# Kernel tuning notes

Measured on AMD Instinct MI355X. Metric: run time of the kernel, lower is better.

The kernel has to match this reference:

```python
import jax, jax.numpy as jnp
import numpy as np

B, S, D, H, L = 2, 4096, 768, 12, 12
DH = D // H
BS = 16                # block size
NB = S // BS           # 256 blocks
NR = 2                 # random blocks per middle query block
DFF = 3072
VOCAB = 50358


def layer_norm(x, s, b):
    m = x.mean(-1, keepdims=True)
    v = ((x - m) ** 2).mean(-1, keepdims=True)
    return (x - m) * jax.lax.rsqrt(v + 1e-12) * s + b


def setup_inputs() -> dict:
    key = jax.random.key(0)
    ks = jax.random.split(key, 20)
    rn = lambda k, shp: jax.random.normal(k, shp, jnp.float32) * 0.02
    # random key-block indices per middle query block, avoiding window+global blocks
    rng = np.random.default_rng(0)
    rb = np.zeros((NB - 2, NR), np.int32)
    for i in range(1, NB - 1):
        forbidden = {0, i - 1, i, i + 1, NB - 1}
        choices = np.array([b for b in range(NB) if b not in forbidden])
        rb[i - 1] = rng.choice(choices, NR, replace=False)
    return {
        "input_ids": jax.random.randint(ks[0], (B, S), 0, VOCAB, jnp.int32),
        "rand_blocks": jnp.asarray(rb),
        "emb_word": rn(ks[1], (VOCAB, D)),
        "emb_pos": rn(ks[2], (S, D)),
        "ln0_s": jnp.ones((D,)), "ln0_b": jnp.zeros((D,)),
        "Wq": rn(ks[3], (L, D, D)), "bq": jnp.zeros((L, D)),
        "Wk": rn(ks[4], (L, D, D)), "bk": jnp.zeros((L, D)),
        "Wv": rn(ks[5], (L, D, D)), "bv": jnp.zeros((L, D)),
        "Wo": rn(ks[6], (L, D, D)), "bo": jnp.zeros((L, D)),
        "ln1_s": jnp.ones((L, D)), "ln1_b": jnp.zeros((L, D)),
        "W1": rn(ks[7], (L, D, DFF)), "b1": jnp.zeros((L, DFF)),
        "W2": rn(ks[8], (L, DFF, D)), "b2": jnp.zeros((L, D)),
        "ln2_s": jnp.ones((L, D)), "ln2_b": jnp.zeros((L, D)),
        "Wp": rn(ks[9], (D, D)), "bp": jnp.zeros((D,)),
        "start_w": jax.random.normal(ks[10], (D,), jnp.float32),
        "end_w": jax.random.normal(ks[11], (D,), jnp.float32),
        "Wd1": rn(ks[12], (D, 20)), "bd1": jnp.zeros((20,)),
        "Wd2": rn(ks[13], (20, 2)), "bd2": jnp.zeros((2,)),
    }


def block_sparse_attn(h, wq, bq_, wk, bk_, wv, bv_, wo, bo_, rand_blocks):
    scale = 1.0 / np.sqrt(DH)
    heads = lambda w, b: (h @ w + b).reshape(B, S, H, DH).transpose(0, 2, 1, 3)
    q = heads(wq, bq_) * scale
    k = heads(wk, bk_)
    v = heads(wv, bv_)
    qb = q.reshape(B, H, NB, BS, DH)
    kb = k.reshape(B, H, NB, BS, DH)
    vb = v.reshape(B, H, NB, BS, DH)
    # global query blocks (first & last) attend to every key
    qg = qb[:, :, jnp.array([0, NB - 1])]                       # [B,H,2,BS,DH]
    ag = jax.nn.softmax(jnp.einsum('bhgqd,bhkd->bhgqk', qg, k), -1)
    og = jnp.einsum('bhgqk,bhkd->bhgqd', ag, v)
    # middle query blocks: global(2) + window(3) + random(2) key blocks
    mid = jnp.arange(1, NB - 1, dtype=jnp.int32)
    idx = jnp.concatenate([
        jnp.zeros((NB - 2, 1), jnp.int32),
        jnp.full((NB - 2, 1), NB - 1, jnp.int32),
        jnp.stack([mid - 1, mid, mid + 1], -1),
        rand_blocks.astype(jnp.int32),
    ], axis=1)                                                  # [NB-2, 7]
    kg = kb[:, :, idx].reshape(B, H, NB - 2, 7 * BS, DH)        # gathered keys
    vg = vb[:, :, idx].reshape(B, H, NB - 2, 7 * BS, DH)
    qm = qb[:, :, 1:NB - 1]                                     # [B,H,NB-2,BS,DH]
    am = jax.nn.softmax(jnp.einsum('bhnqd,bhnkd->bhnqk', qm, kg), -1)
    om = jnp.einsum('bhnqk,bhnkd->bhnqd', am, vg)
    ob = jnp.concatenate([og[:, :, :1], om, og[:, :, 1:]], axis=2)  # [B,H,NB,BS,DH]
    o = ob.reshape(B, H, S, DH).transpose(0, 2, 1, 3).reshape(B, S, D)
    return o @ wo + bo_


def encoder(input_ids, rand_blocks, emb_word, emb_pos, ln0_s, ln0_b,
            Wq, bq, Wk, bk, Wv, bv, Wo, bo, ln1_s, ln1_b,
            W1, b1, W2, b2, ln2_s, ln2_b):
    h = layer_norm(emb_word[input_ids] + emb_pos[None], ln0_s, ln0_b)

    def layer(hc, p):
        wq, bq_, wk, bk_, wv, bv_, wo, bo_, l1s, l1b, w1, b1_, w2, b2_, l2s, l2b = p
        a = block_sparse_attn(hc, wq, bq_, wk, bk_, wv, bv_, wo, bo_, rand_blocks)
        hc = layer_norm(hc + a, l1s, l1b)
        f = jax.nn.gelu(hc @ w1 + b1_, approximate=False) @ w2 + b2_
        hc = layer_norm(hc + f, l2s, l2b)
        return hc, None

    h, _ = jax.lax.scan(layer, h, (Wq, bq, Wk, bk, Wv, bv, Wo, bo,
                                   ln1_s, ln1_b, W1, b1, W2, b2, ln2_s, ln2_b))
    return h


def reference(input_ids, rand_blocks, emb_word, emb_pos, ln0_s, ln0_b,
              Wq, bq, Wk, bk, Wv, bv, Wo, bo, ln1_s, ln1_b,
              W1, b1, W2, b2, ln2_s, ln2_b, Wp, bp,
              start_w, end_w, Wd1, bd1, Wd2, bd2):
    h = encoder(input_ids, rand_blocks, emb_word, emb_pos, ln0_s, ln0_b,
                Wq, bq, Wk, bk, Wv, bv, Wo, bo, ln1_s, ln1_b,
                W1, b1, W2, b2, ln2_s, ln2_b)
    start_logits = h @ start_w        # [B,S]
    end_logits = h @ end_w            # [B,S]
    pooled = jnp.tanh(h[:, 0] @ Wp + bp)   # BERT-style pooler on [CLS]
    d1 = jax.nn.relu(pooled @ Wd1 + bd1)
    disc_logits = d1 @ Wd2 + bd2      # [B,2]
    return start_logits, end_logits, disc_logits
```

## Files before the change

kernel.cpp:

```cpp
#include <hip/hip_runtime.h>

#define DEV __device__ __forceinline__

typedef unsigned short u16;
typedef short bf16x8 __attribute__((ext_vector_type(8)));
typedef float f32x4 __attribute__((ext_vector_type(4)));

constexpr int Bc = 2, Sc = 4096, Dc = 768, Hc = 12, Lc = 12;
constexpr int BSc = 16, NBc = 256, NRc = 2, DFFc = 3072;
constexpr int Mr = Bc * Sc;

DEV u16 f2b(float f) {
  unsigned u = __builtin_bit_cast(unsigned, f);
  u += 0x7fffu + ((u >> 16) & 1u);
  return (u16)(u >> 16);
}
DEV float b2f(u16 u) { return __builtin_bit_cast(float, (unsigned)u << 16); }

DEV void gload_lds16(const void* g, void* l) {
  __builtin_amdgcn_global_load_lds((const __attribute__((address_space(1))) void*)g,
                                   (__attribute__((address_space(3))) void*)l, 16, 0, 0);
}

template<int EPI>
__global__ __launch_bounds__(512, 1)
void gemmP(const u16* __restrict__ A, const u16* __restrict__ Bt,
           const float* __restrict__ bias, u16* __restrict__ Cb,
           float* __restrict__ Cf,
           u16* __restrict__ Qh, u16* __restrict__ Kh, u16* __restrict__ Vh,
           u16* __restrict__ VhT, int M, int N, int K)
{
  __shared__ u16 As[2][128 * 64];
  __shared__ u16 Bs[2][256 * 64];
  const int tid = threadIdx.x;
  const int wid = tid >> 6, lane = tid & 63;
  const int fr = lane & 15, fq = lane >> 4;
  const int wr = wid >> 2, wc = wid & 3;

  int nwg = gridDim.x * gridDim.y;
  int orig = blockIdx.y * gridDim.x + blockIdx.x;
  int swz = (nwg & 7) ? orig : (orig & 7) * (nwg >> 3) + (orig >> 3);
  int bx = swz % gridDim.x, by = swz / gridDim.x;
  const int m0 = by * 128, n0 = bx * 256;

  const u16* asrc[2];
  const u16* bsrc[4];
#pragma unroll
  for (int p = 0; p < 2; ++p) {
    int ci = p * 512 + tid;
    int r = ci >> 3, c = (ci & 7) ^ (r & 7);
    asrc[p] = A + (size_t)(m0 + r) * K + c * 8;
  }
#pragma unroll
  for (int p = 0; p < 4; ++p) {
    int ci = p * 512 + tid;
    int r = ci >> 3, c = (ci & 7) ^ (r & 7);
    bsrc[p] = Bt + (size_t)(n0 + r) * K + c * 8;
  }
  auto stageA = [&](int buf, int k0) {
#pragma unroll
    for (int p = 0; p < 2; ++p)
      gload_lds16(asrc[p] + k0, &As[buf][(p * 512 + tid) * 8]);
  };
  auto stageB = [&](int buf, int k0) {
#pragma unroll
    for (int p = 0; p < 4; ++p)
      gload_lds16(bsrc[p] + k0, &Bs[buf][(p * 512 + tid) * 8]);
  };

  f32x4 acc[4][4] = {};
  const int arow = wr * 64 + fr;
  const int brow = wc * 64 + fr;

  stageA(0, 0);  stageB(0, 0);
  stageA(1, 64); stageB(1, 64);
  asm volatile("s_waitcnt vmcnt(6)" ::: "memory");
  __builtin_amdgcn_sched_barrier(0);
  __builtin_amdgcn_s_barrier();

  const int nt = K >> 6;
  for (int kt = 0; kt < nt; ++kt) {
    const u16* ab = As[kt & 1];
    const u16* bb = Bs[kt & 1];
    bf16x8 aA[2][2], aB[2][2], bA[2][2], bB[2][2];

#pragma unroll
    for (int f = 0; f < 2; ++f)
#pragma unroll
      for (int kh = 0; kh < 2; ++kh) {
        int rowa = arow + f * 16;
        aA[f][kh] = *(const bf16x8*)(ab + rowa * 64 + (((kh * 4 + fq) ^ (rowa & 7)) << 3));
        int rowb = brow + f * 16;
        bA[f][kh] = *(const bf16x8*)(bb + rowb * 64 + (((kh * 4 + fq) ^ (rowb & 7)) << 3));
      }
    __builtin_amdgcn_s_setprio(1);
#pragma unroll
    for (int m = 0; m < 2; ++m)
#pragma unroll
      for (int n = 0; n < 2; ++n)
#pragma unroll
        for (int kh = 0; kh < 2; ++kh)
          acc[m][n] = __builtin_amdgcn_mfma_f32_16x16x32_bf16(aA[m][kh], bA[n][kh], acc[m][n], 0, 0, 0);
    __builtin_amdgcn_s_setprio(0);

#pragma unroll
    for (int f = 0; f < 2; ++f)
#pragma unroll
      for (int kh = 0; kh < 2; ++kh) {
        int rowb = brow + 32 + f * 16;
        bB[f][kh] = *(const bf16x8*)(bb + rowb * 64 + (((kh * 4 + fq) ^ (rowb & 7)) << 3));
      }
    __builtin_amdgcn_s_setprio(1);
#pragma unroll
    for (int m = 0; m < 2; ++m)
#pragma unroll
      for (int n = 0; n < 2; ++n)
#pragma unroll
        for (int kh = 0; kh < 2; ++kh)
          acc[m][n + 2] = __builtin_amdgcn_mfma_f32_16x16x32_bf16(aA[m][kh], bB[n][kh], acc[m][n + 2], 0, 0, 0);
    __builtin_amdgcn_s_setprio(0);
    asm volatile("s_waitcnt lgkmcnt(0)" ::: "memory");
    __builtin_amdgcn_sched_barrier(0);
    __builtin_amdgcn_s_barrier();

    if (kt + 2 < nt) stageB(kt & 1, (kt + 2) * 64);
#pragma unroll
    for (int f = 0; f < 2; ++f)
#pragma unroll
      for (int kh = 0; kh < 2; ++kh) {
        int rowa = arow + 32 + f * 16;
        aB[f][kh] = *(const bf16x8*)(ab + rowa * 64 + (((kh * 4 + fq) ^ (rowa & 7)) << 3));
      }
    __builtin_amdgcn_s_setprio(1);
#pragma unroll
    for (int m = 0; m < 2; ++m)
#pragma unroll
      for (int n = 0; n < 2; ++n)
#pragma unroll
        for (int kh = 0; kh < 2; ++kh)
          acc[m + 2][n] = __builtin_amdgcn_mfma_f32_16x16x32_bf16(aB[m][kh], bA[n][kh], acc[m + 2][n], 0, 0, 0);
    __builtin_amdgcn_s_setprio(0);
    asm volatile("s_waitcnt lgkmcnt(0)" ::: "memory");
    __builtin_amdgcn_sched_barrier(0);
    __builtin_amdgcn_s_barrier();

    if (kt + 2 < nt) stageA(kt & 1, (kt + 2) * 64);
    __builtin_amdgcn_s_setprio(1);
#pragma unroll
    for (int m = 0; m < 2; ++m)
#pragma unroll
      for (int n = 0; n < 2; ++n)
#pragma unroll
        for (int kh = 0; kh < 2; ++kh)
          acc[m + 2][n + 2] = __builtin_amdgcn_mfma_f32_16x16x32_bf16(aB[m][kh], bB[n][kh], acc[m + 2][n + 2], 0, 0, 0);
    __builtin_amdgcn_s_setprio(0);
    if (kt + 1 < nt) {
      if (kt + 2 < nt) asm volatile("s_waitcnt vmcnt(6)" ::: "memory");
      else             asm volatile("s_waitcnt vmcnt(0)" ::: "memory");
      __builtin_amdgcn_sched_barrier(0);
      __builtin_amdgcn_s_barrier();
    }
  }

#pragma unroll
  for (int m = 0; m < 4; ++m) {
#pragma unroll
    for (int n = 0; n < 4; ++n) {
      int col = n0 + wc * 64 + n * 16 + fr;
      float bv = bias[col];
      if constexpr (EPI == 2) {
        int sec = col / 768;
        int c = col - sec * 768;
        int hh = c >> 6, dd = c & 63;
#pragma unroll
        for (int r = 0; r < 4; ++r) {
          int row = m0 + wr * 64 + m * 16 + fq * 4 + r;
          int bb2 = row >> 12, ss = row & 4095;
          size_t bhh = (size_t)(bb2 * Hc + hh);
          u16 val = f2b(acc[m][n][r] + bv);
          if (sec == 0) Qh[(bhh * Sc + ss) * 64 + dd] = val;
          else if (sec == 1) Kh[(bhh * Sc + ss) * 64 + dd] = val;
          else { Vh[(bhh * Sc + ss) * 64 + dd] = val; VhT[(bhh * 64 + dd) * Sc + ss] = val; }
        }
      } else if constexpr (EPI == 1) {
#pragma unroll
        for (int r = 0; r < 4; ++r) {
          int row = m0 + wr * 64 + m * 16 + fq * 4 + r;
          float v = acc[m][n][r] + bv;
          v = 0.5f * v * (1.f + erff(v * 0.70710678118654752f));
          Cb[(size_t)row * N + col] = f2b(v);
        }
      } else {
#pragma unroll
        for (int r = 0; r < 4; ++r) {
          int row = m0 + wr * 64 + m * 16 + fq * 4 + r;
          Cf[(size_t)row * N + col] = acc[m][n][r] + bv;
        }
      }
    }
  }
}

__global__ void wtrans_all(const float* __restrict__ Wq, const float* __restrict__ Wk,
                           const float* __restrict__ Wv, const float* __restrict__ Wo,
                           const float* __restrict__ W1, const float* __restrict__ W2,
                           u16* __restrict__ wqkvT, u16* __restrict__ woT,
                           u16* __restrict__ w1T, u16* __restrict__ w2T)
{
  int bx = blockIdx.x;
  const float* in; u16* out; int K, N, ntx, t; float scale = 1.f;
  if (bx < 576)       { in = Wq; out = wqkvT;           K = 768;  N = 768;  ntx = 24; t = bx;        scale = 0.125f; }
  else if (bx < 1152) { in = Wk; out = wqkvT + 589824;  K = 768;  N = 768;  ntx = 24; t = bx - 576;  }
  else if (bx < 1728) { in = Wv; out = wqkvT + 1179648; K = 768;  N = 768;  ntx = 24; t = bx - 1152; }
  else if (bx < 2304) { in = Wo; out = woT;             K = 768;  N = 768;  ntx = 24; t = bx - 1728; }
  else if (bx < 4608) { in = W1; out = w1T;             K = 768;  N = 3072; ntx = 96; t = bx - 2304; }
  else                { in = W2; out = w2T;             K = 3072; N = 768;  ntx = 24; t = bx - 4608; }
  int n0 = (t % ntx) * 32, k0 = (t / ntx) * 32;
  __shared__ float tl[32][33];
  int tx = threadIdx.x, ty = threadIdx.y;
#pragma unroll
  for (int yy = 0; yy < 32; yy += 8)
    tl[ty + yy][tx] = in[(size_t)(k0 + ty + yy) * N + n0 + tx];
  __syncthreads();
#pragma unroll
  for (int yy = 0; yy < 32; yy += 8)
    out[(size_t)(n0 + ty + yy) * K + k0 + tx] = f2b(tl[tx][ty + yy] * scale);
}

__global__ void pack_bias(const float* __restrict__ bq, const float* __restrict__ bk,
                          const float* __restrict__ bv, float* __restrict__ bqkv)
{
  int i = blockIdx.x * 256 + threadIdx.x;
  if (i >= Lc * 2304) return;
  int l = i / 2304, j = i % 2304;
  float v = (j < 768) ? bq[(size_t)l * 768 + j] * 0.125f
          : (j < 1536) ? bk[(size_t)l * 768 + j - 768]
                       : bv[(size_t)l * 768 + j - 1536];
  bqkv[i] = v;
}

DEV void breduce2(float& a, float& b) {
  __shared__ float ra[4], rbv[4];
  for (int off = 32; off > 0; off >>= 1) {
    a += __shfl_down(a, off);
    b += __shfl_down(b, off);
  }
  int lane = threadIdx.x & 63, wid = threadIdx.x >> 6;
  if (lane == 0) { ra[wid] = a; rbv[wid] = b; }
  __syncthreads();
  a = ra[0] + ra[1] + ra[2] + ra[3];
  b = rbv[0] + rbv[1] + rbv[2] + rbv[3];
}

__global__ __launch_bounds__(256)
void embed_ln(const int* __restrict__ ids, const float* __restrict__ ew,
              const float* __restrict__ ep, const float* __restrict__ gs,
              const float* __restrict__ gb, float* __restrict__ hout, u16* __restrict__ hb)
{
  int row = blockIdx.x;
  int spos = row & (Sc - 1);
  int id = ids[row];
  int tid = threadIdx.x;
  float x[3], sum = 0.f, ss = 0.f;
#pragma unroll
  for (int j = 0; j < 3; ++j) {
    int i = tid + j * 256;
    x[j] = ew[(size_t)id * Dc + i] + ep[(size_t)spos * Dc + i];
    sum += x[j]; ss += x[j] * x[j];
  }
  breduce2(sum, ss);
  float mean = sum * (1.f / Dc);
  float var = ss * (1.f / Dc) - mean * mean;
  float inv = rsqrtf(var + 1e-12f);
#pragma unroll
  for (int j = 0; j < 3; ++j) {
    int i = tid + j * 256;
    float y = (x[j] - mean) * inv * gs[i] + gb[i];
    hout[(size_t)row * Dc + i] = y;
    hb[(size_t)row * Dc + i] = f2b(y);
  }
}

__global__ __launch_bounds__(256)
void ln_res(const float* X, const float* R, const float* gs, const float* gb,
            float* Yf, u16* Yb)
{
  int row = blockIdx.x;
  int tid = threadIdx.x;
  float x[3], sum = 0.f, ss = 0.f;
#pragma unroll
  for (int j = 0; j < 3; ++j) {
    int i = tid + j * 256;
    x[j] = X[(size_t)row * Dc + i] + R[(size_t)row * Dc + i];
    sum += x[j]; ss += x[j] * x[j];
  }
  breduce2(sum, ss);
  float mean = sum * (1.f / Dc);
  float var = ss * (1.f / Dc) - mean * mean;
  float inv = rsqrtf(var + 1e-12f);
#pragma unroll
  for (int j = 0; j < 3; ++j) {
    int i = tid + j * 256;
    float y = (x[j] - mean) * inv * gs[i] + gb[i];
    Yf[(size_t)row * Dc + i] = y;
    Yb[(size_t)row * Dc + i] = f2b(y);
  }
}

__global__ __launch_bounds__(256)
void gattn_flash(const u16* __restrict__ Qh, const u16* __restrict__ Kh,
                 const u16* __restrict__ VhT, float* __restrict__ part)
{
  __shared__ u16 pb[4][16 * 136];
  __shared__ float ob[4][16][64];
  __shared__ float mlb[4][2][16];
  const int kc = blockIdx.x, g = blockIdx.y, bh = blockIdx.z;
  const int wid = threadIdx.x >> 6, lane = threadIdx.x & 63;
  const int fr = lane & 15, fq = lane >> 4;
  const int qrow = g ? (NBc - 1) * BSc : 0;

  const u16* Qb = Qh + ((size_t)bh * Sc + qrow) * 64;
  const u16* Kb = Kh + (size_t)bh * Sc * 64;
  const u16* Vt = VhT + (size_t)bh * 64 * Sc;

  bf16x8 qa0 = *(const bf16x8*)(Qb + fr * 64 + fq * 8);
  bf16x8 qa1 = *(const bf16x8*)(Qb + fr * 64 + 32 + fq * 8);

  float m[4], l[4];
  f32x4 o[4] = {};
#pragma unroll
  for (int r = 0; r < 4; ++r) { m[r] = -3.4e38f; l[r] = 0.f; }

  u16* pbw = pb[wid];
  const int s0w = kc * 256 + wid * 64;

  for (int it = 0; it < 2; ++it) {
    const int sb = s0w + it * 32;
    f32x4 s[2];
#pragma unroll
    for (int t = 0; t < 2; ++t) {
      const u16* kr = Kb + (size_t)(sb + t * 16 + fr) * 64 + fq * 8;
      bf16x8 kb0 = *(const bf16x8*)(kr);
      bf16x8 kb1 = *(const bf16x8*)(kr + 32);
      f32x4 a = {};
      a = __builtin_amdgcn_mfma_f32_16x16x32_bf16(qa0, kb0, a, 0, 0, 0);
      a = __builtin_amdgcn_mfma_f32_16x16x32_bf16(qa1, kb1, a, 0, 0, 0);
      s[t] = a;
    }
#pragma unroll
    for (int r = 0; r < 4; ++r) {
      float pm = fmaxf(s[0][r], s[1][r]);
#pragma unroll
      for (int off = 1; off < 16; off <<= 1) pm = fmaxf(pm, __shfl_xor(pm, off));
      float nm = fmaxf(m[r], pm);
      float sc = __expf(m[r] - nm);
      m[r] = nm;
      float e0 = __expf(s[0][r] - nm), e1 = __expf(s[1][r] - nm);
      float ps = e0 + e1;
#pragma unroll
      for (int off = 1; off < 16; off <<= 1) ps += __shfl_xor(ps, off);
      l[r] = l[r] * sc + ps;
#pragma unroll
      for (int nn = 0; nn < 4; ++nn) o[nn][r] *= sc;
      pbw[(fq * 4 + r) * 136 + fr] = f2b(e0);
      pbw[(fq * 4 + r) * 136 + 16 + fr] = f2b(e1);
    }
    asm volatile("s_waitcnt lgkmcnt(0)" ::: "memory");
    __builtin_amdgcn_sched_barrier(0);
    bf16x8 pa = *(const bf16x8*)(pbw + fr * 136 + fq * 8);
#pragma unroll
    for (int nn = 0; nn < 4; ++nn) {
      bf16x8 vb = *(const bf16x8*)(Vt + (size_t)(nn * 16 + fr) * Sc + sb + fq * 8);
      o[nn] = __builtin_amdgcn_mfma_f32_16x16x32_bf16(pa, vb, o[nn], 0, 0, 0);
    }
  }

#pragma unroll
  for (int nn = 0; nn < 4; ++nn)
#pragma unroll
    for (int r = 0; r < 4; ++r)
      ob[wid][fq * 4 + r][nn * 16 + fr] = o[nn][r];
  if (fr == 0) {
#pragma unroll
    for (int r = 0; r < 4; ++r) {
      mlb[wid][0][fq * 4 + r] = m[r];
      mlb[wid][1][fq * 4 + r] = l[r];
    }
  }
  __syncthreads();

  float* pp = part + (size_t)(((bh * 2 + g) * 16) + kc) * 1056;
  int tid = threadIdx.x;
#pragma unroll
  for (int k = 0; k < 4; ++k) {
    int oidx = tid + k * 256;
    int q = oidx >> 6, d = oidx & 63;
    float M = fmaxf(fmaxf(mlb[0][0][q], mlb[1][0][q]), fmaxf(mlb[2][0][q], mlb[3][0][q]));
    float O = 0.f, L = 0.f;
#pragma unroll
    for (int w = 0; w < 4; ++w) {
      float f = __expf(mlb[w][0][q] - M);
      O += f * ob[w][q][d];
      L += f * mlb[w][1][q];
    }
    pp[q * 64 + d] = O;
    if (d == 0) { pp[1024 + q] = M; pp[1040 + q] = L; }
  }
}

__global__ __launch_bounds__(256)
void gattn_reduce(const float* __restrict__ part, u16* __restrict__ attnb)
{
  int idx = blockIdx.x;
  int bh = idx >> 1, g = idx & 1;
  int b = bh / Hc, h = bh % Hc;
  int tid = threadIdx.x;
  const float* pbase = part + (size_t)idx * 16 * 1056;
#pragma unroll
  for (int k = 0; k < 4; ++k) {
    int oidx = tid + k * 256;
    int q = oidx >> 6, d = oidx & 63;
    float M = -3.4e38f;
#pragma unroll
    for (int c = 0; c < 16; ++c) M = fmaxf(M, pbase[c * 1056 + 1024 + q]);
    float O = 0.f, L = 0.f;
#pragma unroll
    for (int c = 0; c < 16; ++c) {
      float f = __expf(pbase[c * 1056 + 1024 + q] - M);
      O += f * pbase[c * 1056 + q * 64 + d];
      L += f * pbase[c * 1056 + 1040 + q];
    }
    int srow = (g ? (NBc - 1) * BSc : 0) + q;
    attnb[((size_t)(b * Sc + srow)) * Dc + h * 64 + d] = f2b(O / L);
  }
}

__global__ __launch_bounds__(256)
void mid_attn2(const u16* __restrict__ Qh, const u16* __restrict__ Kh,
               const u16* __restrict__ VhT, const int* __restrict__ rb,
               u16* __restrict__ attnb)
{
  __shared__ u16 pb[4][16 * 136];
  const int wid = threadIdx.x >> 6, lane = threadIdx.x & 63;
  const int w = blockIdx.x * 4 + wid;
  const int n = w % 254, bh = w / 254;
  const int b = bh / Hc, h = bh % Hc;
  const int fr = lane & 15, fq = lane >> 4;

  int idx[7];
  idx[0] = 0; idx[1] = NBc - 1; idx[2] = n; idx[3] = n + 1; idx[4] = n + 2;
  idx[5] = rb[n * NRc]; idx[6] = rb[n * NRc + 1];

  const u16* Qb = Qh + ((size_t)bh * Sc + (n + 1) * BSc) * 64;
  const u16* Kb = Kh + (size_t)bh * Sc * 64;
  const u16* Vt = VhT + (size_t)bh * 64 * Sc;

  bf16x8 qa0 = *(const bf16x8*)(Qb + fr * 64 + fq * 8);
  bf16x8 qa1 = *(const bf16x8*)(Qb + fr * 64 + 32 + fq * 8);

  f32x4 s[7];
#pragma unroll
  for (int t = 0; t < 7; ++t) {
    const u16* kr = Kb + ((size_t)idx[t] * BSc + fr) * 64 + fq * 8;
    bf16x8 kb0 = *(const bf16x8*)(kr);
    bf16x8 kb1 = *(const bf16x8*)(kr + 32);
    f32x4 a = {};
    a = __builtin_amdgcn_mfma_f32_16x16x32_bf16(qa0, kb0, a, 0, 0, 0);
    a = __builtin_amdgcn_mfma_f32_16x16x32_bf16(qa1, kb1, a, 0, 0, 0);
    s[t] = a;
  }

  float mx[4], sm[4];
#pragma unroll
  for (int r = 0; r < 4; ++r) {
    mx[r] = s[0][r];
#pragma unroll
    for (int t = 1; t < 7; ++t) mx[r] = fmaxf(mx[r], s[t][r]);
  }
#pragma unroll
  for (int off = 1; off < 16; off <<= 1)
#pragma unroll
    for (int r = 0; r < 4; ++r) mx[r] = fmaxf(mx[r], __shfl_xor(mx[r], off));
#pragma unroll
  for (int r = 0; r < 4; ++r) sm[r] = 0.f;
#pragma unroll
  for (int t = 0; t < 7; ++t)
#pragma unroll
    for (int r = 0; r < 4; ++r) { float e = expf(s[t][r] - mx[r]); s[t][r] = e; sm[r] += e; }
#pragma unroll
  for (int off = 1; off < 16; off <<= 1)
#pragma unroll
    for (int r = 0; r < 4; ++r) sm[r] += __shfl_xor(sm[r], off);
  float inv[4];
#pragma unroll
  for (int r = 0; r < 4; ++r) inv[r] = 1.f / sm[r];

  u16* pbw = pb[wid];
#pragma unroll
  for (int t = 0; t < 7; ++t)
#pragma unroll
    for (int r = 0; r < 4; ++r)
      pbw[(fq * 4 + r) * 136 + t * 16 + fr] = f2b(s[t][r] * inv[r]);
  for (int i = lane; i < 16 * 24; i += 64) {
    int rr = i / 24, cc = 112 + i % 24;
    pbw[rr * 136 + cc] = 0;
  }
  __syncthreads();

  f32x4 o[4] = {};
#pragma unroll
  for (int ks = 0; ks < 4; ++ks) {
    bf16x8 pa = *(const bf16x8*)(pbw + fr * 136 + ks * 32 + fq * 8);
    int t = ks * 2 + (fq >> 1);
    int tt = (t < 7) ? t : 0;
    size_t voff = (size_t)idx[tt] * BSc + (fq & 1) * 8;
#pragma unroll
    for (int nn = 0; nn < 4; ++nn) {
      bf16x8 vb = *(const bf16x8*)(Vt + (size_t)(nn * 16 + fr) * Sc + voff);
      o[nn] = __builtin_amdgcn_mfma_f32_16x16x32_bf16(pa, vb, o[nn], 0, 0, 0);
    }
  }

  size_t rbase = (size_t)b * Sc + (n + 1) * BSc;
#pragma unroll
  for (int nn = 0; nn < 4; ++nn)
#pragma unroll
    for (int r = 0; r < 4; ++r)
      attnb[(rbase + fq * 4 + r) * Dc + h * 64 + nn * 16 + fr] = f2b(o[nn][r]);
}

__global__ __launch_bounds__(256)
void logits_k(const float* __restrict__ h, const float* __restrict__ sw,
              const float* __restrict__ ew, float* __restrict__ out)
{
  int row = blockIdx.x;
  int tid = threadIdx.x;
  float s1 = 0.f, s2 = 0.f;
#pragma unroll
  for (int j = 0; j < 3; ++j) {
    int i = tid + j * 256;
    float x = h[(size_t)row * Dc + i];
    s1 += x * sw[i]; s2 += x * ew[i];
  }
  breduce2(s1, s2);
  if (tid == 0) { out[row] = s1; out[Mr + row] = s2; }
}

__global__ __launch_bounds__(256)
void pooled_k(const float* __restrict__ h, const float* __restrict__ Wp,
              const float* __restrict__ bp, float* __restrict__ pooled)
{
  int b = blockIdx.y, j0 = blockIdx.x * 64;
  int jl = threadIdx.x & 63, kp = threadIdx.x >> 6;
  __shared__ float hr[768];
  __shared__ float part[4][64];
  for (int i = threadIdx.x; i < 768; i += 256) hr[i] = h[(size_t)b * Sc * Dc + i];
  __syncthreads();
  float a0 = 0.f, a1 = 0.f, a2 = 0.f, a3 = 0.f;
  const float* wp = Wp + (size_t)(kp * 192) * 768 + j0 + jl;
  const float* hk = hr + kp * 192;
#pragma unroll 4
  for (int k = 0; k < 192; k += 4) {
    a0 += hk[k]     * wp[(size_t)k * 768];
    a1 += hk[k + 1] * wp[(size_t)(k + 1) * 768];
    a2 += hk[k + 2] * wp[(size_t)(k + 2) * 768];
    a3 += hk[k + 3] * wp[(size_t)(k + 3) * 768];
  }
  part[kp][jl] = a0 + a1 + a2 + a3;
  __syncthreads();
  if (threadIdx.x < 64) {
    float s = part[0][jl] + part[1][jl] + part[2][jl] + part[3][jl] + bp[j0 + jl];
    pooled[b * 768 + j0 + jl] = tanhf(s);
  }
}

__global__ __launch_bounds__(256)
void head2(const float* __restrict__ pooled, const float* __restrict__ Wd1,
           const float* __restrict__ bd1, const float* __restrict__ Wd2,
           const float* __restrict__ bd2, float* __restrict__ out)
{
  __shared__ float pl[1536];
  __shared__ float part[40][6];
  __shared__ float d1[40];
  int tid = threadIdx.x;
  for (int i = tid; i < 1536; i += 256) pl[i] = pooled[i];
  __syncthreads();
  if (tid < 240) {
    int p = tid / 6, s = tid % 6;
    int b = p / 20, u = p % 20;
    float a = 0.f;
    for (int k = s * 128; k < s * 128 + 128; ++k) a += pl[b * 768 + k] * Wd1[(size_t)k * 20 + u];
    part[p][s] = a;
  }
  __syncthreads();
  if (tid < 40) {
    float a = bd1[tid % 20];
#pragma unroll
    for (int s = 0; s < 6; ++s) a += part[tid][s];
    d1[tid] = fmaxf(a, 0.f);
  }
  __syncthreads();
  if (tid < 4) {
    int b = tid >> 1, o = tid & 1;
    float a = bd2[o];
#pragma unroll
    for (int k = 0; k < 20; ++k) a += d1[b * 20 + k] * Wd2[k * 2 + o];
    out[2 * Mr + b * 2 + o] = a;
  }
}

extern "C" void kernel_launch(void* const* d_in, const int* in_sizes, int n_in,
                              void* d_out, int out_size, void* d_ws, size_t ws_size,
                              hipStream_t stream)
{
  (void)in_sizes; (void)n_in; (void)out_size; (void)ws_size;
  const int*   ids   = (const int*)d_in[0];
  const int*   rbp   = (const int*)d_in[1];
  const float* emb_w = (const float*)d_in[2];
  const float* emb_p = (const float*)d_in[3];
  const float* ln0s  = (const float*)d_in[4];
  const float* ln0b  = (const float*)d_in[5];
  const float* Wq    = (const float*)d_in[6];
  const float* bq    = (const float*)d_in[7];
  const float* Wk    = (const float*)d_in[8];
  const float* bk    = (const float*)d_in[9];
  const float* Wv    = (const float*)d_in[10];
  const float* bv    = (const float*)d_in[11];
  const float* Wo    = (const float*)d_in[12];
  const float* bo    = (const float*)d_in[13];
  const float* ln1s  = (const float*)d_in[14];
  const float* ln1b  = (const float*)d_in[15];
  const float* W1    = (const float*)d_in[16];
  const float* b1    = (const float*)d_in[17];
  const float* W2    = (const float*)d_in[18];
  const float* b2    = (const float*)d_in[19];
  const float* ln2s  = (const float*)d_in[20];
  const float* ln2b  = (const float*)d_in[21];
  const float* Wp    = (const float*)d_in[22];
  const float* bp    = (const float*)d_in[23];
  const float* sw    = (const float*)d_in[24];
  const float* ewv   = (const float*)d_in[25];
  const float* Wd1   = (const float*)d_in[26];
  const float* bd1   = (const float*)d_in[27];
  const float* Wd2   = (const float*)d_in[28];
  const float* bd2   = (const float*)d_in[29];
  float* out = (float*)d_out;

  unsigned char* pc = (unsigned char*)d_ws;
  auto carve = [&](size_t bytes) {
    void* r = (void*)pc;
    pc += (bytes + 255) & ~(size_t)255;
    return r;
  };
  u16*   wqkvT = (u16*)carve((size_t)2304 * 768 * 2);
  u16*   woT   = (u16*)carve((size_t)768 * 768 * 2);
  u16*   w1T   = (u16*)carve((size_t)3072 * 768 * 2);
  u16*   w2T   = (u16*)carve((size_t)768 * 3072 * 2);
  float* bqkv  = (float*)carve((size_t)Lc * 2304 * 4);
  float* h     = (float*)carve((size_t)Mr * Dc * 4);
  u16*   hb    = (u16*)carve((size_t)Mr * Dc * 2);
  u16*   Qh    = (u16*)carve((size_t)Mr * Dc * 2);
  u16*   Kh    = (u16*)carve((size_t)Mr * Dc * 2);
  u16*   Vh    = (u16*)carve((size_t)Mr * Dc * 2);
  u16*   VhT   = (u16*)carve((size_t)Mr * Dc * 2);
  u16*   attnb = (u16*)carve((size_t)Mr * Dc * 2);
  float* c0    = (float*)carve((size_t)Mr * Dc * 4);
  float* pool2 = (float*)carve((size_t)Bc * Dc * 4);
  float* m1ws  = (float*)carve((size_t)Mr * DFFc * 2);
  u16*   m1    = (u16*)m1ws;
  float* part  = (float*)((unsigned char*)m1ws + (size_t)13 * 1024 * 1024);

  pack_bias<<<(Lc * 2304 + 255) / 256, 256, 0, stream>>>(bq, bk, bv, bqkv);
  embed_ln<<<Mr, 256, 0, stream>>>(ids, emb_w, emb_p, ln0s, ln0b, h, hb);

  for (int l = 0; l < Lc; ++l) {
    size_t wsq = (size_t)l * 768 * 768, wff = (size_t)l * 768 * 3072;
    wtrans_all<<<6912, dim3(32, 8), 0, stream>>>(Wq + wsq, Wk + wsq, Wv + wsq, Wo + wsq,
                                                 W1 + wff, W2 + wff, wqkvT, woT, w1T, w2T);
    gemmP<2><<<dim3(9, 64), 512, 0, stream>>>(hb, wqkvT, bqkv + (size_t)l * 2304,
                                              nullptr, nullptr, Qh, Kh, Vh, VhT, Mr, 2304, 768);
    gattn_flash<<<dim3(16, 2, Bc * Hc), 256, 0, stream>>>(Qh, Kh, VhT, part);
    gattn_reduce<<<Bc * Hc * 2, 256, 0, stream>>>(part, attnb);
    mid_attn2<<<1524, 256, 0, stream>>>(Qh, Kh, VhT, rbp, attnb);
    gemmP<0><<<dim3(3, 64), 512, 0, stream>>>(attnb, woT, bo + (size_t)l * 768,
                                              nullptr, c0, nullptr, nullptr, nullptr, nullptr,
                                              Mr, 768, 768);
    ln_res<<<Mr, 256, 0, stream>>>(h, c0, ln1s + (size_t)l * 768, ln1b + (size_t)l * 768, h, hb);
    gemmP<1><<<dim3(12, 64), 512, 0, stream>>>(hb, w1T, b1 + (size_t)l * 3072,
                                               m1, nullptr, nullptr, nullptr, nullptr, nullptr,
                                               Mr, 3072, 768);
    gemmP<0><<<dim3(3, 64), 512, 0, stream>>>(m1, w2T, b2 + (size_t)l * 768,
                                              nullptr, c0, nullptr, nullptr, nullptr, nullptr,
                                              Mr, 768, 3072);
    ln_res<<<Mr, 256, 0, stream>>>(h, c0, ln2s + (size_t)l * 768, ln2b + (size_t)l * 768, h, hb);
  }

  logits_k<<<Mr, 256, 0, stream>>>(h, sw, ewv, out);
  pooled_k<<<dim3(12, Bc), 256, 0, stream>>>(h, Wp, bp, pool2);
  head2<<<1, 256, 0, stream>>>(pool2, Wd1, bd1, Wd2, bd2, out);
}
```

Baseline: 3.725 ms.

## Add 128x128 GEMM for N=768 projections, batch weight transposes, merge attention kernels

Result: no change. 3.703 ms (-0.6%).

```diff
diff --git a/kernel.cpp b/kernel.cpp
--- a/kernel.cpp
+++ b/kernel.cpp
@@ -201,6 +201,153 @@
   }
 }
 
+__global__ __launch_bounds__(256, 2)
+void gemmQ(const u16* __restrict__ A, const u16* __restrict__ Bt,
+           const float* __restrict__ bias, float* __restrict__ Cf,
+           int M, int N, int K)
+{
+  __shared__ u16 As[2][128 * 64];
+  __shared__ u16 Bs[2][128 * 64];
+  const int tid = threadIdx.x;
+  const int wid = tid >> 6, lane = tid & 63;
+  const int fr = lane & 15, fq = lane >> 4;
+  const int wr = wid >> 1, wc = wid & 1;
+
+  int nwg = gridDim.x * gridDim.y;
+  int orig = blockIdx.y * gridDim.x + blockIdx.x;
+  int swz = (nwg & 7) ? orig : (orig & 7) * (nwg >> 3) + (orig >> 3);
+  int bx = swz % gridDim.x, by = swz / gridDim.x;
+  const int m0 = by * 128, n0 = bx * 128;
+
+  const u16* asrc[4];
+  const u16* bsrc[4];
+#pragma unroll
+  for (int p = 0; p < 4; ++p) {
+    int ci = p * 256 + tid;
+    int r = ci >> 3, c = (ci & 7) ^ (r & 7);
+    asrc[p] = A + (size_t)(m0 + r) * K + c * 8;
+    bsrc[p] = Bt + (size_t)(n0 + r) * K + c * 8;
+  }
+  auto stageA = [&](int buf, int k0) {
+#pragma unroll
+    for (int p = 0; p < 4; ++p)
+      gload_lds16(asrc[p] + k0, &As[buf][(p * 256 + tid) * 8]);
+  };
+  auto stageB = [&](int buf, int k0) {
+#pragma unroll
+    for (int p = 0; p < 4; ++p)
+      gload_lds16(bsrc[p] + k0, &Bs[buf][(p * 256 + tid) * 8]);
+  };
+
+  f32x4 acc[4][4] = {};
+  const int arow = wr * 64 + fr;
+  const int brow = wc * 64 + fr;
+
+  stageA(0, 0);  stageB(0, 0);
+  stageA(1, 64); stageB(1, 64);
+  asm volatile("s_waitcnt vmcnt(8)" ::: "memory");
+  __builtin_amdgcn_sched_barrier(0);
+  __builtin_amdgcn_s_barrier();
+
+  const int nt = K >> 6;
+  for (int kt = 0; kt < nt; ++kt) {
+    const u16* ab = As[kt & 1];
+    const u16* bb = Bs[kt & 1];
+    bf16x8 aA[2][2], aB[2][2], bA[2][2], bB[2][2];
+
+#pragma unroll
+    for (int f = 0; f < 2; ++f)
+#pragma unroll
+      for (int kh = 0; kh < 2; ++kh) {
+        int rowa = arow + f * 16;
+        aA[f][kh] = *(const bf16x8*)(ab + rowa * 64 + (((kh * 4 + fq) ^ (rowa & 7)) << 3));
+        int rowb = brow + f * 16;
+        bA[f][kh] = *(const bf16x8*)(bb + rowb * 64 + (((kh * 4 + fq) ^ (rowb & 7)) << 3));
+      }
+    __builtin_amdgcn_s_setprio(1);
+#pragma unroll
+    for (int m = 0; m < 2; ++m)
+#pragma unroll
+      for (int n = 0; n < 2; ++n)
+#pragma unroll
+        for (int kh = 0; kh < 2; ++kh)
+          acc[m][n] = __builtin_amdgcn_mfma_f32_16x16x32_bf16(aA[m][kh], bA[n][kh], acc[m][n], 0, 0, 0);
+    __builtin_amdgcn_s_setprio(0);
+
+#pragma unroll
+    for (int f = 0; f < 2; ++f)
+#pragma unroll
+      for (int kh = 0; kh < 2; ++kh) {
+        int rowb = brow + 32 + f * 16;
+        bB[f][kh] = *(const bf16x8*)(bb + rowb * 64 + (((kh * 4 + fq) ^ (rowb & 7)) << 3));
+      }
+    __builtin_amdgcn_s_setprio(1);
+#pragma unroll
+    for (int m = 0; m < 2; ++m)
+#pragma unroll
+      for (int n = 0; n < 2; ++n)
+#pragma unroll
+        for (int kh = 0; kh < 2; ++kh)
+          acc[m][n + 2] = __builtin_amdgcn_mfma_f32_16x16x32_bf16(aA[m][kh], bB[n][kh], acc[m][n + 2], 0, 0, 0);
+    __builtin_amdgcn_s_setprio(0);
+    asm volatile("s_waitcnt lgkmcnt(0)" ::: "memory");
+    __builtin_amdgcn_sched_barrier(0);
+    __builtin_amdgcn_s_barrier();
+
+    if (kt + 2 < nt) stageB(kt & 1, (kt + 2) * 64);
+#pragma unroll
+    for (int f = 0; f < 2; ++f)
+#pragma unroll
+      for (int kh = 0; kh < 2; ++kh) {
+        int rowa = arow + 32 + f * 16;
+        aB[f][kh] = *(const bf16x8*)(ab + rowa * 64 + (((kh * 4 + fq) ^ (rowa & 7)) << 3));
+      }
+    __builtin_amdgcn_s_setprio(1);
+#pragma unroll
+    for (int m = 0; m < 2; ++m)
+#pragma unroll
+      for (int n = 0; n < 2; ++n)
+#pragma unroll
+        for (int kh = 0; kh < 2; ++kh)
+          acc[m + 2][n] = __builtin_amdgcn_mfma_f32_16x16x32_bf16(aB[m][kh], bA[n][kh], acc[m + 2][n], 0, 0, 0);
+    __builtin_amdgcn_s_setprio(0);
+    asm volatile("s_waitcnt lgkmcnt(0)" ::: "memory");
+    __builtin_amdgcn_sched_barrier(0);
+    __builtin_amdgcn_s_barrier();
+
+    if (kt + 2 < nt) stageA(kt & 1, (kt + 2) * 64);
+    __builtin_amdgcn_s_setprio(1);
+#pragma unroll
+    for (int m = 0; m < 2; ++m)
+#pragma unroll
+      for (int n = 0; n < 2; ++n)
+#pragma unroll
+        for (int kh = 0; kh < 2; ++kh)
+          acc[m + 2][n + 2] = __builtin_amdgcn_mfma_f32_16x16x32_bf16(aB[m][kh], bB[n][kh], acc[m + 2][n + 2], 0, 0, 0);
+    __builtin_amdgcn_s_setprio(0);
+    if (kt + 1 < nt) {
+      if (kt + 2 < nt) asm volatile("s_waitcnt vmcnt(8)" ::: "memory");
+      else             asm volatile("s_waitcnt vmcnt(0)" ::: "memory");
+      __builtin_amdgcn_sched_barrier(0);
+      __builtin_amdgcn_s_barrier();
+    }
+  }
+
+#pragma unroll
+  for (int m = 0; m < 4; ++m) {
+#pragma unroll
+    for (int n = 0; n < 4; ++n) {
+      int col = n0 + wc * 64 + n * 16 + fr;
+      float bv = bias[col];
+#pragma unroll
+      for (int r = 0; r < 4; ++r) {
+        int row = m0 + wr * 64 + m * 16 + fq * 4 + r;
+        Cf[(size_t)row * N + col] = acc[m][n][r] + bv;
+      }
+    }
+  }
+}
+
 __global__ void wtrans_all(const float* __restrict__ Wq, const float* __restrict__ Wk,
                            const float* __restrict__ Wv, const float* __restrict__ Wo,
                            const float* __restrict__ W1, const float* __restrict__ W2,
@@ -208,13 +355,15 @@
                            u16* __restrict__ w1T, u16* __restrict__ w2T)
 {
   int bx = blockIdx.x;
+  size_t l = blockIdx.y;
+  size_t wsq = l * 768 * 768, wff = l * 768 * 3072;
   const float* in; u16* out; int K, N, ntx, t; float scale = 1.f;
-  if (bx < 576)       { in = Wq; out = wqkvT;           K = 768;  N = 768;  ntx = 24; t = bx;        scale = 0.125f; }
-  else if (bx < 1152) { in = Wk; out = wqkvT + 589824;  K = 768;  N = 768;  ntx = 24; t = bx - 576;  }
-  else if (bx < 1728) { in = Wv; out = wqkvT + 1179648; K = 768;  N = 768;  ntx = 24; t = bx - 1152; }
-  else if (bx < 2304) { in = Wo; out = woT;             K = 768;  N = 768;  ntx = 24; t = bx - 1728; }
-  else if (bx < 4608) { in = W1; out = w1T;             K = 768;  N = 3072; ntx = 96; t = bx - 2304; }
-  else                { in = W2; out = w2T;             K = 3072; N = 768;  ntx = 24; t = bx - 4608; }
+  if (bx < 576)       { in = Wq + wsq; out = wqkvT + l * 2304 * 768;           K = 768;  N = 768;  ntx = 24; t = bx;        scale = 0.125f; }
+  else if (bx < 1152) { in = Wk + wsq; out = wqkvT + l * 2304 * 768 + 589824;  K = 768;  N = 768;  ntx = 24; t = bx - 576;  }
+  else if (bx < 1728) { in = Wv + wsq; out = wqkvT + l * 2304 * 768 + 1179648; K = 768;  N = 768;  ntx = 24; t = bx - 1152; }
+  else if (bx < 2304) { in = Wo + wsq; out = woT + l * 768 * 768;              K = 768;  N = 768;  ntx = 24; t = bx - 1728; }
+  else if (bx < 4608) { in = W1 + wff; out = w1T + l * 3072 * 768;             K = 768;  N = 3072; ntx = 96; t = bx - 2304; }
+  else                { in = W2 + wff; out = w2T + l * 768 * 3072;             K = 3072; N = 768;  ntx = 24; t = bx - 4608; }
   int n0 = (t % ntx) * 32, k0 = (t / ntx) * 32;
   __shared__ float tl[32][33];
   int tx = threadIdx.x, ty = threadIdx.y;
@@ -409,40 +558,39 @@
 }
 
 __global__ __launch_bounds__(256)
-void gattn_reduce(const float* __restrict__ part, u16* __restrict__ attnb)
-{
-  int idx = blockIdx.x;
-  int bh = idx >> 1, g = idx & 1;
-  int b = bh / Hc, h = bh % Hc;
-  int tid = threadIdx.x;
-  const float* pbase = part + (size_t)idx * 16 * 1056;
-#pragma unroll
-  for (int k = 0; k < 4; ++k) {
-    int oidx = tid + k * 256;
-    int q = oidx >> 6, d = oidx & 63;
-    float M = -3.4e38f;
-#pragma unroll
-    for (int c = 0; c < 16; ++c) M = fmaxf(M, pbase[c * 1056 + 1024 + q]);
-    float O = 0.f, L = 0.f;
-#pragma unroll
-    for (int c = 0; c < 16; ++c) {
-      float f = __expf(pbase[c * 1056 + 1024 + q] - M);
-      O += f * pbase[c * 1056 + q * 64 + d];
-      L += f * pbase[c * 1056 + 1040 + q];
-    }
-    int srow = (g ? (NBc - 1) * BSc : 0) + q;
-    attnb[((size_t)(b * Sc + srow)) * Dc + h * 64 + d] = f2b(O / L);
-  }
-}
-
-__global__ __launch_bounds__(256)
-void mid_attn2(const u16* __restrict__ Qh, const u16* __restrict__ Kh,
+void attn_tail(const u16* __restrict__ Qh, const u16* __restrict__ Kh,
                const u16* __restrict__ VhT, const int* __restrict__ rb,
-               u16* __restrict__ attnb)
-{
+               const float* __restrict__ part, u16* __restrict__ attnb)
+{
+  if (blockIdx.x < 48) {
+    int idx = blockIdx.x;
+    int bh = idx >> 1, g = idx & 1;
+    int b = bh / Hc, h = bh % Hc;
+    int tid = threadIdx.x;
+    const float* pbase = part + (size_t)idx * 16 * 1056;
+#pragma unroll
+    for (int k = 0; k < 4; ++k) {
+      int oidx = tid + k * 256;
+      int q = oidx >> 6, d = oidx & 63;
+      float M = -3.4e38f;
+#pragma unroll
+      for (int c = 0; c < 16; ++c) M = fmaxf(M, pbase[c * 1056 + 1024 + q]);
+      float O = 0.f, L = 0.f;
+#pragma unroll
+      for (int c = 0; c < 16; ++c) {
+        float f = __expf(pbase[c * 1056 + 1024 + q] - M);
+        O += f * pbase[c * 1056 + q * 64 + d];
+        L += f * pbase[c * 1056 + 1040 + q];
+      }
+      int srow = (g ? (NBc - 1) * BSc : 0) + q;
+      attnb[((size_t)(b * Sc + srow)) * Dc + h * 64 + d] = f2b(O / L);
+    }
+    return;
+  }
+
   __shared__ u16 pb[4][16 * 136];
   const int wid = threadIdx.x >> 6, lane = threadIdx.x & 63;
-  const int w = blockIdx.x * 4 + wid;
+  const int w = (blockIdx.x - 48) * 4 + wid;
   const int n = w % 254, bh = w / 254;
   const int b = bh / Hc, h = bh % Hc;
   const int fr = lane & 15, fq = lane >> 4;
@@ -652,10 +800,10 @@
     pc += (bytes + 255) & ~(size_t)255;
     return r;
   };
-  u16*   wqkvT = (u16*)carve((size_t)2304 * 768 * 2);
-  u16*   woT   = (u16*)carve((size_t)768 * 768 * 2);
-  u16*   w1T   = (u16*)carve((size_t)3072 * 768 * 2);
-  u16*   w2T   = (u16*)carve((size_t)768 * 3072 * 2);
+  u16*   wqkvT = (u16*)carve((size_t)Lc * 2304 * 768 * 2);
+  u16*   woT   = (u16*)carve((size_t)Lc * 768 * 768 * 2);
+  u16*   w1T   = (u16*)carve((size_t)Lc * 3072 * 768 * 2);
+  u16*   w2T   = (u16*)carve((size_t)Lc * 768 * 3072 * 2);
   float* bqkv  = (float*)carve((size_t)Lc * 2304 * 4);
   float* h     = (float*)carve((size_t)Mr * Dc * 4);
   u16*   hb    = (u16*)carve((size_t)Mr * Dc * 2);
@@ -671,27 +819,25 @@
   float* part  = (float*)((unsigned char*)m1ws + (size_t)13 * 1024 * 1024);
 
   pack_bias<<<(Lc * 2304 + 255) / 256, 256, 0, stream>>>(bq, bk, bv, bqkv);
+  wtrans_all<<<dim3(6912, Lc), dim3(32, 8), 0, stream>>>(Wq, Wk, Wv, Wo, W1, W2,
+                                                         wqkvT, woT, w1T, w2T);
   embed_ln<<<Mr, 256, 0, stream>>>(ids, emb_w, emb_p, ln0s, ln0b, h, hb);
 
   for (int l = 0; l < Lc; ++l) {
-    size_t wsq = (size_t)l * 768 * 768, wff = (size_t)l * 768 * 3072;
-    wtrans_all<<<6912, dim3(32, 8), 0, stream>>>(Wq + wsq, Wk + wsq, Wv + wsq, Wo + wsq,
-                                                 W1 + wff, W2 + wff, wqkvT, woT, w1T, w2T);
-    gemmP<2><<<dim3(9, 64), 512, 0, stream>>>(hb, wqkvT, bqkv + (size_t)l * 2304,
+    gemmP<2><<<dim3(9, 64), 512, 0, stream>>>(hb, wqkvT + (size_t)l * 2304 * 768,
+                                              bqkv + (size_t)l * 2304,
                                               nullptr, nullptr, Qh, Kh, Vh, VhT, Mr, 2304, 768);
     gattn_flash<<<dim3(16, 2, Bc * Hc), 256, 0, stream>>>(Qh, Kh, VhT, part);
-    gattn_reduce<<<Bc * Hc * 2, 256, 0, stream>>>(part, attnb);
-    mid_attn2<<<1524, 256, 0, stream>>>(Qh, Kh, VhT, rbp, attnb);
-    gemmP<0><<<dim3(3, 64), 512, 0, stream>>>(attnb, woT, bo + (size_t)l * 768,
-                                              nullptr, c0, nullptr, nullptr, nullptr, nullptr,
-                                              Mr, 768, 768);
+    attn_tail<<<48 + 1524, 256, 0, stream>>>(Qh, Kh, VhT, rbp, part, attnb);
+    gemmQ<<<dim3(6, 64), 256, 0, stream>>>(attnb, woT + (size_t)l * 768 * 768,
+                                           bo + (size_t)l * 768, c0, Mr, 768, 768);
     ln_res<<<Mr, 256, 0, stream>>>(h, c0, ln1s + (size_t)l * 768, ln1b + (size_t)l * 768, h, hb);
-    gemmP<1><<<dim3(12, 64), 512, 0, stream>>>(hb, w1T, b1 + (size_t)l * 3072,
+    gemmP<1><<<dim3(12, 64), 512, 0, stream>>>(hb, w1T + (size_t)l * 3072 * 768,
+                                               b1 + (size_t)l * 3072,
                                                m1, nullptr, nullptr, nullptr, nullptr, nullptr,
                                                Mr, 3072, 768);
-    gemmP<0><<<dim3(3, 64), 512, 0, stream>>>(m1, w2T, b2 + (size_t)l * 768,
-                                              nullptr, c0, nullptr, nullptr, nullptr, nullptr,
-                                              Mr, 768, 3072);
+    gemmQ<<<dim3(6, 64), 256, 0, stream>>>(m1, w2T + (size_t)l * 768 * 3072,
+                                           b2 + (size_t)l * 768, c0, Mr, 768, 3072);
     ln_res<<<Mr, 256, 0, stream>>>(h, c0, ln2s + (size_t)l * 768, ln2b + (size_t)l * 768, h, hb);
   }
 
```
